# Kernel tuning notes

Measured on AMD Instinct MI355X. Metric: run time of the kernel, lower is better.

Reference implementation:

```python
import jax, jax.numpy as jnp
import numpy as np

N, E, NC = 50000, 800000, 5
H, C = 4, 16      # branch GATConvs: heads=4, out=16 -> 64
H2, C2 = 4, 32    # conv2/conv3: heads=4, out=32 -> 128
HID = 128


def _gat(x, src, dst, W, a_s, a_d, b, mask=None, edge_attr=None, We=None, a_e=None):
    """PyG-style GATConv with add_self_loops=True (fill_value='mean' for edge_attr)."""
    n = x.shape[0]
    h, c = a_s.shape
    hx = (x @ W).reshape(n, h, c)                      # [N,H,C]
    as_n = (hx * a_s).sum(-1)                          # [N,H]
    ad_n = (hx * a_d).sum(-1)                          # [N,H]
    alpha = as_n[src] + ad_n[dst]                      # [E,H]
    loop = as_n + ad_n                                 # self-loop scores [N,H]
    if edge_attr is not None:
        ee = (edge_attr @ We).reshape(-1, h, c)        # [E,H,C]
        alpha = alpha + (ee * a_e).sum(-1)
        w = mask.astype(x.dtype) if mask is not None else jnp.ones((edge_attr.shape[0],), x.dtype)
        # fill_value='mean': self-loop attr = mean of (masked) incoming edge_attr
        loop_attr = jax.ops.segment_sum(edge_attr * w[:, None], dst, n) / \
                    jnp.maximum(jax.ops.segment_sum(w, dst, n), 1.0)[:, None]
        loop = loop + ((loop_attr @ We).reshape(n, h, c) * a_e).sum(-1)
    alpha = jax.nn.leaky_relu(alpha, 0.2)
    loop = jax.nn.leaky_relu(loop, 0.2)
    if mask is not None:
        alpha = jnp.where(mask[:, None], alpha, -jnp.inf)
    # segment softmax over destination neighborhoods (self-loop always present)
    m = jnp.maximum(jax.ops.segment_max(alpha, dst, n), loop)      # [N,H], finite
    ex = jnp.exp(alpha - m[dst])                                   # [E,H]
    if mask is not None:
        ex = jnp.where(mask[:, None], ex, 0.0)
    exl = jnp.exp(loop - m)                                        # [N,H]
    denom = jax.ops.segment_sum(ex, dst, n) + exl
    out = jax.ops.segment_sum(ex[:, :, None] * hx[src], dst, n) + exl[:, :, None] * hx
    return (out / denom[:, :, None]).reshape(n, h * c) + b


def setup_inputs() -> dict:
    key = jax.random.key(0)
    ks = iter(jax.random.split(key, 64))
    def nrm(shape, s=0.1):
        return jax.random.normal(next(ks), shape, jnp.float32) * s
    d = {}
    d["x"] = nrm((N, 1), 1.0)
    d["edge_index"] = jax.random.randint(next(ks), (2, E), 0, N, jnp.int32)
    d["edge_attr"] = nrm((E, 3), 1.0)
    d["mask_t"] = jax.random.randint(next(ks), (E,), 0, 2, jnp.int32).astype(bool)
    d["mask_g"] = jax.random.randint(next(ks), (E,), 0, 2, jnp.int32).astype(bool)
    d["mask_p"] = jax.random.randint(next(ks), (E,), 0, 2, jnp.int32).astype(bool)
    for p in ("t", "g", "p"):
        d[f"W{p}"] = nrm((1, H * C))
        d[f"a{p}s"] = nrm((H, C)); d[f"a{p}d"] = nrm((H, C)); d[f"a{p}e"] = nrm((H, C))
        d[f"W{p}e"] = nrm((3, H * C))
        d[f"b{p}"] = jnp.zeros((H * C,), jnp.float32)
    d["Wf"] = nrm((3 * H * C, HID)); d["bf"] = jnp.zeros((HID,), jnp.float32)
    d["W2"] = nrm((HID, H2 * C2)); d["a2s"] = nrm((H2, C2)); d["a2d"] = nrm((H2, C2)); d["b2"] = jnp.zeros((H2 * C2,), jnp.float32)
    d["W3"] = nrm((HID, H2 * C2)); d["a3s"] = nrm((H2, C2)); d["a3d"] = nrm((H2, C2)); d["b3"] = jnp.zeros((H2 * C2,), jnp.float32)
    d["Wc1"] = nrm((HID, HID // 2)); d["bc1"] = jnp.zeros((HID // 2,), jnp.float32)
    d["Wc2"] = nrm((HID // 2, NC)); d["bc2"] = jnp.zeros((NC,), jnp.float32)
    return d


def reference(x, edge_index, edge_attr, mask_t, mask_g, mask_p,
              Wt, ats, atd, ate, Wte, bt,
              Wg, ags, agd, age, Wge, bg,
              Wp, aps, apd, ape, Wpe, bp,
              Wf, bf, W2, a2s, a2d, b2, W3, a3s, a3d, b3,
              Wc1, bc1, Wc2, bc2):
    src, dst = edge_index[0], edge_index[1]
    ht = _gat(x, src, dst, Wt, ats, atd, bt, mask_t, edge_attr, Wte, ate)
    hg = _gat(x, src, dst, Wg, ags, agd, bg, mask_g, edge_attr, Wge, age)
    hp = _gat(x, src, dst, Wp, aps, apd, bp, mask_p, edge_attr, Wpe, ape)
    h = jax.nn.relu(jnp.concatenate([ht, hg, hp], -1) @ Wf + bf)
    h = jax.nn.relu(_gat(h, src, dst, W2, a2s, a2d, b2))
    h = jax.nn.relu(_gat(h, src, dst, W3, a3s, a3d, b3))
    logits = jax.nn.relu(h @ Wc1 + bc1) @ Wc2 + bc2
    return jax.nn.log_softmax(logits, -1)
```

## Files before the change

### kernel.cpp

```cpp
#include <hip/hip_runtime.h>
#include <hip/hip_bf16.h>

#define LEAKY(v) ((v) > 0.f ? (v) : 0.2f * (v))

typedef __attribute__((ext_vector_type(8))) short s8;
typedef __attribute__((ext_vector_type(4))) float f4;
typedef __attribute__((ext_vector_type(4))) unsigned short us4;

__device__ __forceinline__ unsigned short f_to_bf16(float f) {
    union { float f; unsigned int i; } v; v.f = f;
    unsigned int x = v.i;
    return (unsigned short)((x + 0x7fffu + ((x >> 16) & 1u)) >> 16);
}

__device__ __forceinline__ float2 bf2_to_f2(unsigned int u) {
    union { unsigned int i; float f; } a, b;
    a.i = (u & 0xffffu) << 16;
    b.i = u & 0xffff0000u;
    float2 r; r.x = a.f; r.y = b.f;
    return r;
}

struct ConstBuf {
    float ws[3][4];
    float wd[3][4];
    float M[3][3][4];
    float G[12][128];
    float bias2[128];
};
#define CB_FLOATS 1724

struct BranchW { const float *W, *as_, *ad_, *ae, *We, *b; };
struct PreArgs { BranchW br[3]; const float *Wf, *bf; ConstBuf* cb; };

__global__ void k_pre_all(PreArgs A, const float* __restrict__ W2, unsigned short* __restrict__ wf2,
                          const float* __restrict__ W3, unsigned short* __restrict__ wf3) {
    int t = threadIdx.x;
    if (blockIdx.x == 0) {
        if (t < 24) {
            int b = t / 8, r = t % 8, h = r & 3; bool isd = r >= 4;
            const float* a = isd ? A.br[b].ad_ : A.br[b].as_;
            float s = 0.f;
            for (int c = 0; c < 16; ++c) s += A.br[b].W[h * 16 + c] * a[h * 16 + c];
            if (isd) A.cb->wd[b][h] = s; else A.cb->ws[b][h] = s;
        }
        if (t >= 32 && t < 68) {
            int id = t - 32, b = id / 12, k = (id % 12) / 4, h = id & 3;
            float s = 0.f;
            for (int c = 0; c < 16; ++c) s += A.br[b].We[k * 64 + h * 16 + c] * A.br[b].ae[h * 16 + c];
            A.cb->M[b][k][h] = s;
        }
        if (t >= 128) {
            int j = t - 128;
            float s = A.bf[j];
            for (int b = 0; b < 3; ++b)
                for (int i = 0; i < 64; ++i)
                    s += A.br[b].b[i] * A.Wf[(b * 64 + i) * 128 + j];
            A.cb->bias2[j] = s;
        }
        for (int id = t; id < 1536; id += 256) {
            int r = id >> 7, j = id & 127, b = r >> 2, h = r & 3;
            float s = 0.f;
            for (int c = 0; c < 16; ++c)
                s += A.br[b].W[h * 16 + c] * A.Wf[(b * 64 + h * 16 + c) * 128 + j];
            A.cb->G[r][j] = s;
        }
    } else {
        const float* W = (blockIdx.x == 1) ? W2 : W3;
        unsigned short* out = (blockIdx.x == 1) ? wf2 : wf3;
        for (int i = t; i < 16384; i += 256) {
            int j = i & 7, lane = (i >> 3) & 63, kk = (i >> 9) & 3, ct = i >> 11;
            int k = kk * 32 + (lane >> 4) * 8 + j;
            int n = ct * 16 + (lane & 15);
            out[i] = f_to_bf16(W[k * 128 + n]);
        }
    }
}

__global__ void k_count(const int* __restrict__ ei, int E, int* __restrict__ deg) {
    int e = blockIdx.x * blockDim.x + threadIdx.x;
    if (e < E) atomicAdd(&deg[ei[E + e]], 1);
}

#define SCAN_EPB 2048

__global__ void k_scan1(const int* __restrict__ deg, int* __restrict__ off,
                        int* __restrict__ partials, int total) {
    __shared__ int sd[256];
    int t = threadIdx.x;
    int base = blockIdx.x * SCAN_EPB + t * 8;
    int v[8];
    int s = 0;
    #pragma unroll
    for (int i = 0; i < 8; ++i) {
        int idx = base + i;
        v[i] = (idx < total - 1) ? deg[idx] : 0;
        s += v[i];
    }
    sd[t] = s;
    __syncthreads();
    #pragma unroll
    for (int ofs = 1; ofs < 256; ofs <<= 1) {
        int u = (t >= ofs) ? sd[t - ofs] : 0;
        __syncthreads();
        sd[t] += u;
        __syncthreads();
    }
    if (t == 255) partials[blockIdx.x] = sd[255];
    int run = sd[t] - s;
    #pragma unroll
    for (int i = 0; i < 8; ++i) {
        int idx = base + i;
        if (idx < total) off[idx] = run;
        run += v[i];
    }
}

__global__ void k_scan2(int* __restrict__ partials, int nb) {
    __shared__ int sd[256];
    int t = threadIdx.x;
    int v = (t < nb) ? partials[t] : 0;
    sd[t] = v;
    __syncthreads();
    #pragma unroll
    for (int ofs = 1; ofs < 256; ofs <<= 1) {
        int u = (t >= ofs) ? sd[t - ofs] : 0;
        __syncthreads();
        sd[t] += u;
        __syncthreads();
    }
    if (t < nb) partials[t] = sd[t] - v;
}

__global__ void k_scan3(int* __restrict__ off, const int* __restrict__ partials,
                        int* __restrict__ cursor, int total) {
    int idx = blockIdx.x * blockDim.x + threadIdx.x;
    if (idx < total) {
        int v = off[idx] + partials[idx / SCAN_EPB];
        off[idx] = v;
        if (idx < total - 1) cursor[idx] = v;
    }
}

__global__ void k_scatter(const int* __restrict__ ei, const float* __restrict__ attr,
                          const int* __restrict__ mt, const int* __restrict__ mg,
                          const int* __restrict__ mp, int E, int chunk,
                          int* __restrict__ cursor, float4* __restrict__ rec) {
    int r = blockIdx.x & 7;
    int slice = blockIdx.x >> 3;
    int e = slice * 256 + threadIdx.x;
    if (e >= E) return;
    int d = ei[E + e];
    if ((unsigned)(d - r * chunk) >= (unsigned)chunk) return;
    int p = atomicAdd(&cursor[d], 1);
    float4 rr;
    rr.x = attr[e * 3 + 0];
    rr.y = attr[e * 3 + 1];
    rr.z = attr[e * 3 + 2];
    unsigned int bits = (mt[e] != 0 ? 1u : 0u) | (mg[e] != 0 ? 2u : 0u) | (mp[e] != 0 ? 4u : 0u);
    rr.w = __int_as_float((int)((unsigned)ei[e] | (bits << 16)));
    rec[p] = rr;
}

__global__ void k_branch(const float* __restrict__ x, const int* __restrict__ off,
                         const float4* __restrict__ rec, int* __restrict__ csr_src,
                         const ConstBuf* __restrict__ cb, float* __restrict__ h1, int N) {
    __shared__ float sc[CB_FLOATS];
    for (int i = threadIdx.x; i < CB_FLOATS; i += 256) sc[i] = ((const float*)cb)[i];
    __syncthreads();
    int g = threadIdx.x >> 4, l = threadIdx.x & 15;
    int n = blockIdx.x * 16 + g;
    if (n >= N) return;

    float num[12], den[12], asum[9], cnt[3];
    #pragma unroll
    for (int i = 0; i < 12; ++i) { num[i] = 0.f; den[i] = 0.f; }
    #pragma unroll
    for (int i = 0; i < 9; ++i) asum[i] = 0.f;
    cnt[0] = cnt[1] = cnt[2] = 0.f;

    float xn = x[n];
    int beg = off[n], end = off[n + 1];
    for (int p = beg + l; p < end; p += 16) {
        float4 r = rec[p];
        unsigned int packed = (unsigned int)__float_as_int(r.w);
        int src = (int)(packed & 0xffffu);
        unsigned int bits = packed >> 16;
        csr_src[p] = src;
        float xs = x[src];
        float a0 = r.x, a1 = r.y, a2 = r.z;
        #pragma unroll
        for (int b = 0; b < 3; ++b) {
            if ((bits >> b) & 1u) {
                cnt[b] += 1.f;
                asum[b * 3 + 0] += a0; asum[b * 3 + 1] += a1; asum[b * 3 + 2] += a2;
                #pragma unroll
                for (int h = 0; h < 4; ++h) {
                    float al = xs * sc[b * 4 + h] + xn * sc[12 + b * 4 + h]
                             + a0 * sc[24 + b * 12 + 0 + h]
                             + a1 * sc[24 + b * 12 + 4 + h]
                             + a2 * sc[24 + b * 12 + 8 + h];
                    al = LEAKY(al);
                    float ex = __expf(al);
                    den[b * 4 + h] += ex;
                    num[b * 4 + h] += ex * xs;
                }
            }
        }
    }
    #pragma unroll
    for (int m = 1; m < 16; m <<= 1) {
        #pragma unroll
        for (int i = 0; i < 12; ++i) {
            num[i] += __shfl_xor(num[i], m, 64);
            den[i] += __shfl_xor(den[i], m, 64);
        }
        #pragma unroll
        for (int i = 0; i < 9; ++i) asum[i] += __shfl_xor(asum[i], m, 64);
        #pragma unroll
        for (int i = 0; i < 3; ++i) cnt[i] += __shfl_xor(cnt[i], m, 64);
    }
    float S[12];
    #pragma unroll
    for (int b = 0; b < 3; ++b) {
        float inv = 1.f / fmaxf(cnt[b], 1.f);
        float l0 = asum[b * 3 + 0] * inv, l1 = asum[b * 3 + 1] * inv, l2 = asum[b * 3 + 2] * inv;
        #pragma unroll
        for (int h = 0; h < 4; ++h) {
            float lp = xn * (sc[b * 4 + h] + sc[12 + b * 4 + h])
                     + l0 * sc[24 + b * 12 + 0 + h]
                     + l1 * sc[24 + b * 12 + 4 + h]
                     + l2 * sc[24 + b * 12 + 8 + h];
            lp = LEAKY(lp);
            float exl = __expf(lp);
            float sden = den[b * 4 + h] + exl;
            S[b * 4 + h] = (num[b * 4 + h] + exl * xn) / sden;
        }
    }
    int jb = l * 8;
    float o[8];
    #pragma unroll
    for (int q = 0; q < 8; ++q) {
        int j = jb + q;
        float a = sc[60 + 1536 + j];
        #pragma unroll
        for (int k = 0; k < 12; ++k) a += S[k] * sc[60 + k * 128 + j];
        o[q] = fmaxf(a, 0.f);
    }
    float4* dst = (float4*)(h1 + (size_t)n * 128 + jb);
    dst[0] = make_float4(o[0], o[1], o[2], o[3]);
    dst[1] = make_float4(o[4], o[5], o[6], o[7]);
}

__global__ void k_mm128b(const float* __restrict__ A, const unsigned short* __restrict__ wf,
                         unsigned short* __restrict__ hxb, int N) {
    __shared__ unsigned short sA[64 * 136];
    __shared__ unsigned short sW[16384];
    int tid = threadIdx.x;
    int base = blockIdx.x * 64;
    const float4* wf4 = (const float4*)wf;
    float4* sW4 = (float4*)sW;
    #pragma unroll
    for (int i = 0; i < 8; ++i) sW4[tid + i * 256] = wf4[tid + i * 256];
    #pragma unroll
    for (int i = 0; i < 8; ++i) {
        int f = tid + i * 256;
        int row = f >> 5, c4 = f & 31;
        int n = base + row;
        float4 v = (n < N) ? ((const float4*)A)[(size_t)n * 32 + c4]
                           : make_float4(0.f, 0.f, 0.f, 0.f);
        us4 b;
        b.x = f_to_bf16(v.x); b.y = f_to_bf16(v.y);
        b.z = f_to_bf16(v.z); b.w = f_to_bf16(v.w);
        *(us4*)(&sA[row * 136 + c4 * 4]) = b;
    }
    __syncthreads();
    int wv = tid >> 6, lane = tid & 63;
    int q = lane >> 4, l15 = lane & 15;
    int rowbase = wv * 16;
    s8 af[4];
    #pragma unroll
    for (int kk = 0; kk < 4; ++kk)
        af[kk] = *(const s8*)(&sA[(rowbase + l15) * 136 + kk * 32 + q * 8]);
    #pragma unroll
    for (int ct = 0; ct < 8; ++ct) {
        f4 acc = {0.f, 0.f, 0.f, 0.f};
        #pragma unroll
        for (int kk = 0; kk < 4; ++kk) {
            s8 bfr = *(const s8*)(&sW[((ct * 4 + kk) * 64 + lane) * 8]);
            acc = __builtin_amdgcn_mfma_f32_16x16x32_bf16(af[kk], bfr, acc, 0, 0, 0);
        }
        #pragma unroll
        for (int r = 0; r < 4; ++r) {
            int n = base + rowbase + q * 4 + r;
            if (n < N) hxb[(size_t)n * 128 + ct * 16 + l15] = f_to_bf16(acc[r]);
        }
    }
}

__global__ void k_scoresb(const unsigned short* __restrict__ hxb, const float* __restrict__ a_s,
                          const float* __restrict__ a_d, float* __restrict__ as_,
                          float* __restrict__ ad_, int N) {
    __shared__ float sas[128], sad[128];
    if (threadIdx.x < 128) { sas[threadIdx.x] = a_s[threadIdx.x]; sad[threadIdx.x] = a_d[threadIdx.x]; }
    __syncthreads();
    int tid = blockIdx.x * blockDim.x + threadIdx.x;
    int n = tid >> 2, h = tid & 3;
    if (n >= N) return;
    const uint4* r4 = (const uint4*)(hxb + (size_t)n * 128 + h * 32);
    float ss = 0.f, sd2 = 0.f;
    #pragma unroll
    for (int c = 0; c < 4; ++c) {
        uint4 blob = r4[c];
        unsigned int us[4] = { blob.x, blob.y, blob.z, blob.w };
        #pragma unroll
        for (int q = 0; q < 4; ++q) {
            float2 v = bf2_to_f2(us[q]);
            int col = h * 32 + c * 8 + q * 2;
            ss  += v.x * sas[col] + v.y * sas[col + 1];
            sd2 += v.x * sad[col] + v.y * sad[col + 1];
        }
    }
    as_[(size_t)n * 4 + h] = ss;
    ad_[(size_t)n * 4 + h] = sd2;
}

__global__ void k_gatagg(const unsigned short* __restrict__ hxb, const float* __restrict__ as_,
                         const float* __restrict__ ad_, const float* __restrict__ b,
                         const int* __restrict__ off, const int* __restrict__ csr_src,
                         float* __restrict__ out, int N) {
    int wave = threadIdx.x >> 6, lane = threadIdx.x & 63;
    int n = blockIdx.x * 4 + wave;
    if (n >= N) return;
    int h = lane >> 4;
    int lofs = lane * 2;
    float adn = ad_[(size_t)n * 4 + h];
    int beg = off[n], end = off[n + 1];
    float acc0 = 0.f, acc1 = 0.f, accd = 0.f;
    for (int p = beg; p < end; p += 16) {
        int s[16]; float e[16]; unsigned int u[16]; bool valid[16];
        #pragma unroll
        for (int i = 0; i < 16; ++i) {
            valid[i] = (p + i < end);
            int q = valid[i] ? (p + i) : beg;
            s[i] = csr_src[q];
        }
        #pragma unroll
        for (int i = 0; i < 16; ++i) e[i] = as_[(size_t)s[i] * 4 + h];
        #pragma unroll
        for (int i = 0; i < 16; ++i) u[i] = *(const unsigned int*)(hxb + (size_t)s[i] * 128 + lofs);
        #pragma unroll
        for (int i = 0; i < 16; ++i) {
            float ex = valid[i] ? __expf(LEAKY(e[i] + adn)) : 0.f;
            float2 v = bf2_to_f2(u[i]);
            acc0 += ex * v.x; acc1 += ex * v.y; accd += ex;
        }
    }
    float aln = LEAKY(as_[(size_t)n * 4 + h] + adn);
    float exl = __expf(aln);
    unsigned int un = *(const unsigned int*)(hxb + (size_t)n * 128 + lofs);
    float2 vn = bf2_to_f2(un);
    float inv = 1.f / (accd + exl);
    float o0 = (acc0 + exl * vn.x) * inv + b[lofs + 0];
    float o1 = (acc1 + exl * vn.y) * inv + b[lofs + 1];
    float2 r; r.x = fmaxf(o0, 0.f); r.y = fmaxf(o1, 0.f);
    *(float2*)(out + (size_t)n * 128 + lofs) = r;
}

#define CLS_NPB 32
__global__ void k_cls(const float* __restrict__ h3, const float* __restrict__ Wc1,
                      const float* __restrict__ bc1, const float* __restrict__ Wc2,
                      const float* __restrict__ bc2, float* __restrict__ out, int N) {
    __shared__ float hs[CLS_NPB * 128];
    int tid = threadIdx.x;
    int nb = blockIdx.x * CLS_NPB;
    for (int i = tid; i < CLS_NPB * 128; i += 256) {
        int n = nb + (i >> 7);
        hs[i] = (n < N) ? h3[(size_t)n * 128 + (i & 127)] : 0.f;
    }
    __syncthreads();
    int g = tid >> 6, j = tid & 63;
    const float4* hb4 = (const float4*)(hs + g * 8 * 128);
    float bj = bc1[j];
    float acc[8];
    #pragma unroll
    for (int i = 0; i < 8; ++i) acc[i] = bj;
    for (int k = 0; k < 128; k += 4) {
        float w0 = Wc1[(k + 0) * 64 + j];
        float w1 = Wc1[(k + 1) * 64 + j];
        float w2 = Wc1[(k + 2) * 64 + j];
        float w3 = Wc1[(k + 3) * 64 + j];
        #pragma unroll
        for (int i = 0; i < 8; ++i) {
            float4 h4 = hb4[(i * 128 + k) >> 2];
            acc[i] += h4.x * w0 + h4.y * w1 + h4.z * w2 + h4.w * w3;
        }
    }
    float w2v[5];
    #pragma unroll
    for (int c = 0; c < 5; ++c) w2v[c] = Wc2[j * 5 + c];
    #pragma unroll
    for (int i = 0; i < 8; ++i) {
        float t = fmaxf(acc[i], 0.f);
        float p[5];
        #pragma unroll
        for (int c = 0; c < 5; ++c) p[c] = t * w2v[c];
        #pragma unroll
        for (int m = 1; m < 64; m <<= 1) {
            #pragma unroll
            for (int c = 0; c < 5; ++c) p[c] += __shfl_xor(p[c], m, 64);
        }
        if (j == 0) {
            int n = nb + g * 8 + i;
            if (n < N) {
                float l[5], mx = -1e30f;
                #pragma unroll
                for (int c = 0; c < 5; ++c) { l[c] = p[c] + bc2[c]; mx = fmaxf(mx, l[c]); }
                float s = 0.f;
                #pragma unroll
                for (int c = 0; c < 5; ++c) s += __expf(l[c] - mx);
                float lse = mx + __logf(s);
                #pragma unroll
                for (int c = 0; c < 5; ++c) out[(size_t)n * 5 + c] = l[c] - lse;
            }
        }
    }
}

extern "C" void kernel_launch(void* const* d_in, const int* in_sizes, int n_in,
                              void* d_out, int out_size, void* d_ws, size_t ws_size,
                              hipStream_t stream) {
    const float* x    = (const float*)d_in[0];
    const int*   ei   = (const int*)d_in[1];
    const float* attr = (const float*)d_in[2];
    const int*   mt   = (const int*)d_in[3];
    const int*   mg   = (const int*)d_in[4];
    const int*   mp   = (const int*)d_in[5];
    const float* Wf   = (const float*)d_in[24];
    const float* bf   = (const float*)d_in[25];
    const float* W2   = (const float*)d_in[26];
    const float* a2s  = (const float*)d_in[27];
    const float* a2d  = (const float*)d_in[28];
    const float* b2   = (const float*)d_in[29];
    const float* W3   = (const float*)d_in[30];
    const float* a3s  = (const float*)d_in[31];
    const float* a3d  = (const float*)d_in[32];
    const float* b3   = (const float*)d_in[33];
    const float* Wc1  = (const float*)d_in[34];
    const float* bc1  = (const float*)d_in[35];
    const float* Wc2  = (const float*)d_in[36];
    const float* bc2  = (const float*)d_in[37];

    int N = in_sizes[0];
    int E = in_sizes[1] / 2;

    char* w = (char*)d_ws;
    auto alloc = [&](size_t bytes) {
        char* p = w;
        w += (bytes + 255) & ~(size_t)255;
        return p;
    };
    int* off      = (int*)alloc((size_t)(N + 1) * 4);
    int* cursor   = (int*)alloc((size_t)N * 4);
    int* deg      = (int*)alloc((size_t)N * 4);
    int* partials = (int*)alloc(1024 * 4);
    int* csr_src  = (int*)alloc((size_t)E * 4);
    ConstBuf* cb  = (ConstBuf*)alloc(sizeof(ConstBuf));
    float* as_    = (float*)alloc((size_t)N * 4 * 4);
    float* ad_    = (float*)alloc((size_t)N * 4 * 4);
    float* bufA   = (float*)alloc((size_t)N * 128 * 4);
    float4* rec   = (float4*)alloc((size_t)E * 16);
    unsigned short* hxb = (unsigned short*)alloc((size_t)N * 256);
    unsigned short* wf2 = (unsigned short*)alloc(16384 * 2);
    unsigned short* wf3 = (unsigned short*)alloc(16384 * 2);

    PreArgs pa;
    for (int b = 0; b < 3; ++b) {
        pa.br[b].W   = (const float*)d_in[6 + b * 6 + 0];
        pa.br[b].as_ = (const float*)d_in[6 + b * 6 + 1];
        pa.br[b].ad_ = (const float*)d_in[6 + b * 6 + 2];
        pa.br[b].ae  = (const float*)d_in[6 + b * 6 + 3];
        pa.br[b].We  = (const float*)d_in[6 + b * 6 + 4];
        pa.br[b].b   = (const float*)d_in[6 + b * 6 + 5];
    }
    pa.Wf = Wf; pa.bf = bf; pa.cb = cb;

    int total = N + 1;
    int nScanBlocks = (total + SCAN_EPB - 1) / SCAN_EPB;

    hipMemsetAsync(deg, 0, (size_t)N * 4, stream);
    hipLaunchKernelGGL(k_pre_all, dim3(3), dim3(256), 0, stream, pa, W2, wf2, W3, wf3);
    int gE = (E + 255) / 256;
    hipLaunchKernelGGL(k_count, dim3(gE), dim3(256), 0, stream, ei, E, deg);
    hipLaunchKernelGGL(k_scan1, dim3(nScanBlocks), dim3(256), 0, stream, deg, off, partials, total);
    hipLaunchKernelGGL(k_scan2, dim3(1), dim3(256), 0, stream, partials, nScanBlocks);
    hipLaunchKernelGGL(k_scan3, dim3((total + 255) / 256), dim3(256), 0, stream,
                       off, partials, cursor, total);
    int chunk = (N + 7) / 8;
    hipLaunchKernelGGL(k_scatter, dim3(gE * 8), dim3(256), 0, stream,
                       ei, attr, mt, mg, mp, E, chunk, cursor, rec);
    hipLaunchKernelGGL(k_branch, dim3((N + 15) / 16), dim3(256), 0, stream,
                       x, off, rec, csr_src, cb, bufA, N);
    hipLaunchKernelGGL(k_mm128b, dim3((N + 63) / 64), dim3(256), 0, stream,
                       bufA, wf2, hxb, N);
    hipLaunchKernelGGL(k_scoresb, dim3(((size_t)N * 4 + 255) / 256), dim3(256), 0, stream,
                       hxb, a2s, a2d, as_, ad_, N);
    hipLaunchKernelGGL(k_gatagg, dim3((N + 3) / 4), dim3(256), 0, stream,
                       hxb, as_, ad_, b2, off, csr_src, bufA, N);
    hipLaunchKernelGGL(k_mm128b, dim3((N + 63) / 64), dim3(256), 0, stream,
                       bufA, wf3, hxb, N);
    hipLaunchKernelGGL(k_scoresb, dim3(((size_t)N * 4 + 255) / 256), dim3(256), 0, stream,
                       hxb, a3s, a3d, as_, ad_, N);
    hipLaunchKernelGGL(k_gatagg, dim3((N + 3) / 4), dim3(256), 0, stream,
                       hxb, as_, ad_, b3, off, csr_src, bufA, N);
    hipLaunchKernelGGL(k_cls, dim3((N + CLS_NPB - 1) / CLS_NPB), dim3(256), 0, stream,
                       bufA, Wc1, bc1, Wc2, bc2, (float*)d_out, N);
}
```

Baseline: 454.6 us.

## Fuse attention scores into matmul, merge memset/scan2, cooperative edge gather in gatagg

Computes the per-head source and destination attention scores inside the MFMA matmul epilogue using fp32 accumulators and cross-lane shuffles, which removes the separate score kernel and its re-read of the bf16 features. The degree-buffer memset moves into the preprocessing kernel, and the separate partial-scan kernel is replaced by a serial per-thread prefix loop in the offset kernel, cutting launches. In the aggregation kernel, each lane loads one edge index and computes one head's exp, then broadcasts them via shuffles instead of every lane redundantly loading all indices and scores. Risks are more shuffle and register traffic in the matmul and a small redundant loop over partials per thread.

```diff
diff --git a/kernel.cpp b/kernel.cpp
--- a/kernel.cpp
+++ b/kernel.cpp
@@ -34,7 +34,8 @@
 struct PreArgs { BranchW br[3]; const float *Wf, *bf; ConstBuf* cb; };
 
 __global__ void k_pre_all(PreArgs A, const float* __restrict__ W2, unsigned short* __restrict__ wf2,
-                          const float* __restrict__ W3, unsigned short* __restrict__ wf3) {
+                          const float* __restrict__ W3, unsigned short* __restrict__ wf3,
+                          int* __restrict__ deg, int N) {
     int t = threadIdx.x;
     if (blockIdx.x == 0) {
         if (t < 24) {
@@ -65,7 +66,7 @@
                 s += A.br[b].W[h * 16 + c] * A.Wf[(b * 64 + h * 16 + c) * 128 + j];
             A.cb->G[r][j] = s;
         }
-    } else {
+    } else if (blockIdx.x <= 2) {
         const float* W = (blockIdx.x == 1) ? W2 : W3;
         unsigned short* out = (blockIdx.x == 1) ? wf2 : wf3;
         for (int i = t; i < 16384; i += 256) {
@@ -74,6 +75,9 @@
             int n = ct * 16 + (lane & 15);
             out[i] = f_to_bf16(W[k * 128 + n]);
         }
+    } else {
+        int idx = (blockIdx.x - 3) * 256 + t;
+        if (idx < N) deg[idx] = 0;
     }
 }
 
@@ -116,27 +120,14 @@
     }
 }
 
-__global__ void k_scan2(int* __restrict__ partials, int nb) {
-    __shared__ int sd[256];
-    int t = threadIdx.x;
-    int v = (t < nb) ? partials[t] : 0;
-    sd[t] = v;
-    __syncthreads();
-    #pragma unroll
-    for (int ofs = 1; ofs < 256; ofs <<= 1) {
-        int u = (t >= ofs) ? sd[t - ofs] : 0;
-        __syncthreads();
-        sd[t] += u;
-        __syncthreads();
-    }
-    if (t < nb) partials[t] = sd[t] - v;
-}
-
 __global__ void k_scan3(int* __restrict__ off, const int* __restrict__ partials,
                         int* __restrict__ cursor, int total) {
     int idx = blockIdx.x * blockDim.x + threadIdx.x;
     if (idx < total) {
-        int v = off[idx] + partials[idx / SCAN_EPB];
+        int pb = idx / SCAN_EPB;
+        int addv = 0;
+        for (int j = 0; j < pb; ++j) addv += partials[j];
+        int v = off[idx] + addv;
         off[idx] = v;
         if (idx < total - 1) cursor[idx] = v;
     }
@@ -253,7 +244,9 @@
 }
 
 __global__ void k_mm128b(const float* __restrict__ A, const unsigned short* __restrict__ wf,
-                         unsigned short* __restrict__ hxb, int N) {
+                         const float* __restrict__ a_s, const float* __restrict__ a_d,
+                         unsigned short* __restrict__ hxb, float* __restrict__ as_,
+                         float* __restrict__ ad_, int N) {
     __shared__ unsigned short sA[64 * 136];
     __shared__ unsigned short sW[16384];
     int tid = threadIdx.x;
@@ -282,6 +275,14 @@
     #pragma unroll
     for (int kk = 0; kk < 4; ++kk)
         af[kk] = *(const s8*)(&sA[(rowbase + l15) * 136 + kk * 32 + q * 8]);
+    float as8[8], ad8[8];
+    #pragma unroll
+    for (int ct = 0; ct < 8; ++ct) { as8[ct] = a_s[ct * 16 + l15]; ad8[ct] = a_d[ct * 16 + l15]; }
+    float ss[4][4], sdd[4][4];
+    #pragma unroll
+    for (int r = 0; r < 4; ++r)
+        #pragma unroll
+        for (int hh = 0; hh < 4; ++hh) { ss[r][hh] = 0.f; sdd[r][hh] = 0.f; }
     #pragma unroll
     for (int ct = 0; ct < 8; ++ct) {
         f4 acc = {0.f, 0.f, 0.f, 0.f};
@@ -290,39 +291,39 @@
             s8 bfr = *(const s8*)(&sW[((ct * 4 + kk) * 64 + lane) * 8]);
             acc = __builtin_amdgcn_mfma_f32_16x16x32_bf16(af[kk], bfr, acc, 0, 0, 0);
         }
+        int hh = ct >> 1;
+        float asv = as8[ct], adv = ad8[ct];
         #pragma unroll
         for (int r = 0; r < 4; ++r) {
             int n = base + rowbase + q * 4 + r;
             if (n < N) hxb[(size_t)n * 128 + ct * 16 + l15] = f_to_bf16(acc[r]);
-        }
-    }
-}
-
-__global__ void k_scoresb(const unsigned short* __restrict__ hxb, const float* __restrict__ a_s,
-                          const float* __restrict__ a_d, float* __restrict__ as_,
-                          float* __restrict__ ad_, int N) {
-    __shared__ float sas[128], sad[128];
-    if (threadIdx.x < 128) { sas[threadIdx.x] = a_s[threadIdx.x]; sad[threadIdx.x] = a_d[threadIdx.x]; }
-    __syncthreads();
-    int tid = blockIdx.x * blockDim.x + threadIdx.x;
-    int n = tid >> 2, h = tid & 3;
-    if (n >= N) return;
-    const uint4* r4 = (const uint4*)(hxb + (size_t)n * 128 + h * 32);
-    float ss = 0.f, sd2 = 0.f;
-    #pragma unroll
-    for (int c = 0; c < 4; ++c) {
-        uint4 blob = r4[c];
-        unsigned int us[4] = { blob.x, blob.y, blob.z, blob.w };
-        #pragma unroll
-        for (int q = 0; q < 4; ++q) {
-            float2 v = bf2_to_f2(us[q]);
-            int col = h * 32 + c * 8 + q * 2;
-            ss  += v.x * sas[col] + v.y * sas[col + 1];
-            sd2 += v.x * sad[col] + v.y * sad[col + 1];
-        }
-    }
-    as_[(size_t)n * 4 + h] = ss;
-    ad_[(size_t)n * 4 + h] = sd2;
+            ss[r][hh] += acc[r] * asv;
+            sdd[r][hh] += acc[r] * adv;
+        }
+    }
+    #pragma unroll
+    for (int m = 1; m < 16; m <<= 1) {
+        #pragma unroll
+        for (int r = 0; r < 4; ++r)
+            #pragma unroll
+            for (int hh = 0; hh < 4; ++hh) {
+                ss[r][hh] += __shfl_xor(ss[r][hh], m, 64);
+                sdd[r][hh] += __shfl_xor(sdd[r][hh], m, 64);
+            }
+    }
+    #pragma unroll
+    for (int hh = 0; hh < 4; ++hh) {
+        if (l15 == hh) {
+            #pragma unroll
+            for (int r = 0; r < 4; ++r) {
+                int n = base + rowbase + q * 4 + r;
+                if (n < N) {
+                    as_[(size_t)n * 4 + hh] = ss[r][hh];
+                    ad_[(size_t)n * 4 + hh] = sdd[r][hh];
+                }
+            }
+        }
+    }
 }
 
 __global__ void k_gatagg(const unsigned short* __restrict__ hxb, const float* __restrict__ as_,
@@ -334,25 +335,24 @@
     if (n >= N) return;
     int h = lane >> 4;
     int lofs = lane * 2;
+    int hm = lane & 3;
+    int im = lane >> 2;
     float adn = ad_[(size_t)n * 4 + h];
+    float adnm = ad_[(size_t)n * 4 + hm];
     int beg = off[n], end = off[n + 1];
     float acc0 = 0.f, acc1 = 0.f, accd = 0.f;
     for (int p = beg; p < end; p += 16) {
-        int s[16]; float e[16]; unsigned int u[16]; bool valid[16];
+        int pm = p + im;
+        bool vm = pm < end;
+        int sm = csr_src[vm ? pm : beg];
+        float em = as_[(size_t)sm * 4 + hm];
+        float exm = vm ? __expf(LEAKY(em + adnm)) : 0.f;
         #pragma unroll
         for (int i = 0; i < 16; ++i) {
-            valid[i] = (p + i < end);
-            int q = valid[i] ? (p + i) : beg;
-            s[i] = csr_src[q];
-        }
-        #pragma unroll
-        for (int i = 0; i < 16; ++i) e[i] = as_[(size_t)s[i] * 4 + h];
-        #pragma unroll
-        for (int i = 0; i < 16; ++i) u[i] = *(const unsigned int*)(hxb + (size_t)s[i] * 128 + lofs);
-        #pragma unroll
-        for (int i = 0; i < 16; ++i) {
-            float ex = valid[i] ? __expf(LEAKY(e[i] + adn)) : 0.f;
-            float2 v = bf2_to_f2(u[i]);
+            int sb = __shfl(sm, i * 4, 64);
+            float ex = __shfl(exm, i * 4 + h, 64);
+            unsigned int u = *(const unsigned int*)(hxb + (size_t)sb * 128 + lofs);
+            float2 v = bf2_to_f2(u);
             acc0 += ex * v.x; acc1 += ex * v.y; accd += ex;
         }
     }
@@ -488,12 +488,11 @@
     int total = N + 1;
     int nScanBlocks = (total + SCAN_EPB - 1) / SCAN_EPB;
 
-    hipMemsetAsync(deg, 0, (size_t)N * 4, stream);
-    hipLaunchKernelGGL(k_pre_all, dim3(3), dim3(256), 0, stream, pa, W2, wf2, W3, wf3);
+    hipLaunchKernelGGL(k_pre_all, dim3(3 + (N + 255) / 256), dim3(256), 0, stream,
+                       pa, W2, wf2, W3, wf3, deg, N);
     int gE = (E + 255) / 256;
     hipLaunchKernelGGL(k_count, dim3(gE), dim3(256), 0, stream, ei, E, deg);
     hipLaunchKernelGGL(k_scan1, dim3(nScanBlocks), dim3(256), 0, stream, deg, off, partials, total);
-    hipLaunchKernelGGL(k_scan2, dim3(1), dim3(256), 0, stream, partials, nScanBlocks);
     hipLaunchKernelGGL(k_scan3, dim3((total + 255) / 256), dim3(256), 0, stream,
                        off, partials, cursor, total);
     int chunk = (N + 7) / 8;
@@ -502,15 +501,11 @@
     hipLaunchKernelGGL(k_branch, dim3((N + 15) / 16), dim3(256), 0, stream,
                        x, off, rec, csr_src, cb, bufA, N);
     hipLaunchKernelGGL(k_mm128b, dim3((N + 63) / 64), dim3(256), 0, stream,
-                       bufA, wf2, hxb, N);
-    hipLaunchKernelGGL(k_scoresb, dim3(((size_t)N * 4 + 255) / 256), dim3(256), 0, stream,
-                       hxb, a2s, a2d, as_, ad_, N);
+                       bufA, wf2, a2s, a2d, hxb, as_, ad_, N);
     hipLaunchKernelGGL(k_gatagg, dim3((N + 3) / 4), dim3(256), 0, stream,
                        hxb, as_, ad_, b2, off, csr_src, bufA, N);
     hipLaunchKernelGGL(k_mm128b, dim3((N + 63) / 64), dim3(256), 0, stream,
-                       bufA, wf3, hxb, N);
-    hipLaunchKernelGGL(k_scoresb, dim3(((size_t)N * 4 + 255) / 256), dim3(256), 0, stream,
-                       hxb, a3s, a3d, as_, ad_, N);
+                       bufA, wf3, a3s, a3d, hxb, as_, ad_, N);
     hipLaunchKernelGGL(k_gatagg, dim3((N + 3) / 4), dim3(256), 0, stream,
                        hxb, as_, ad_, b3, off, csr_src, bufA, N);
     hipLaunchKernelGGL(k_cls, dim3((N + CLS_NPB - 1) / CLS_NPB), dim3(256), 0, stream,
```

Measured after the change: 438.4 us. -3.6%, faster.
